# Optimization experiments

Hardware: AMD Instinct MI355X
Metric: run time of the kernel (lower is better)

## Reference

```python
import jax, jax.numpy as jnp
import numpy as np

D_K = 1024
NHEADS = 16
HEAD_DIM = D_K // NHEADS  # 64
STD = float(np.sqrt(HEAD_DIM))  # matches math.sqrt(d_k // nheads)


def setup_inputs() -> dict:
    key = jax.random.key(0)
    ks = jax.random.split(key, 9)
    B, S = 2, 2048
    scale = 1.0 / np.sqrt(D_K)
    x = jax.random.normal(ks[0], (B, S, D_K), dtype=jnp.float32)
    Wq = jax.random.normal(ks[1], (D_K, D_K), dtype=jnp.float32) * scale
    bq = jnp.zeros((D_K,), dtype=jnp.float32)
    Wk = jax.random.normal(ks[2], (D_K, D_K), dtype=jnp.float32) * scale
    bk = jnp.zeros((D_K,), dtype=jnp.float32)
    Wv = jax.random.normal(ks[3], (D_K, D_K), dtype=jnp.float32) * scale
    bv = jnp.zeros((D_K,), dtype=jnp.float32)
    Wo = jax.random.normal(ks[4], (D_K, D_K), dtype=jnp.float32) * scale
    bo = jnp.zeros((D_K,), dtype=jnp.float32)
    return {"x": x, "Wq": Wq, "bq": bq, "Wk": Wk, "bk": bk,
            "Wv": Wv, "bv": bv, "Wo": Wo, "bo": bo}


def _heads(x, W, b):
    # Linear then split heads: (B,S,D) -> (B,H,S,hd)
    B, S, _ = x.shape
    out = x @ W.T + b
    return out.reshape(B, S, NHEADS, HEAD_DIM).transpose(0, 2, 1, 3)


def reference(x, Wq, bq, Wk, bk, Wv, bv, Wo, bo):
    B, S, _ = x.shape
    q = _heads(x, Wq, bq)  # (B,H,S,hd)
    k = _heads(x, Wk, bk)
    v = _heads(x, Wv, bv)
    scores = jnp.einsum('bhqd,bhkd->bhqk', q, k) / STD  # (B,H,S,S)
    causal = jnp.tril(jnp.ones((S, S), dtype=bool))  # mask_factory default
    scores = jnp.where(causal[None, None, :, :], scores, -jnp.inf)
    attn = jax.nn.softmax(scores, axis=-1)
    ctx = jnp.einsum('bhqk,bhkd->bhqd', attn, v)  # (B,H,S,hd)
    ctx = ctx.transpose(0, 2, 1, 3).reshape(B, S, D_K)
    return ctx @ Wo.T + bo
```

## Files before the change

kernel.cpp:

```cpp
#include <hip/hip_runtime.h>
#include <stdint.h>

typedef unsigned short u16;
typedef __bf16 bf16x8 __attribute__((ext_vector_type(8)));
typedef __bf16 bf16x4v __attribute__((ext_vector_type(4)));
typedef float f32x4 __attribute__((ext_vector_type(4)));

typedef __attribute__((address_space(3))) uint32_t lds_u32;
typedef __attribute__((address_space(1))) uint32_t glb_u32;

__device__ __forceinline__ f32x4 mfma16(bf16x8 a, bf16x8 b, f32x4 c) {
    return __builtin_amdgcn_mfma_f32_16x16x32_bf16(a, b, c, 0, 0, 0);
}

__device__ __forceinline__ ushort4 pk4(float a, float b, float c, float d) {
    bf16x4v v;
    v[0] = (__bf16)a; v[1] = (__bf16)b; v[2] = (__bf16)c; v[3] = (__bf16)d;
    union { bf16x4v v; ushort4 u; } cv; cv.v = v; return cv.u;
}

__device__ __forceinline__ float fexp2(float x) {
    return __builtin_amdgcn_exp2f(x);
}

__device__ __forceinline__ void async16(const u16* g, u16* l) {
    __builtin_amdgcn_global_load_lds((glb_u32*)(uintptr_t)(const void*)g,
                                     (lds_u32*)l, 16, 0, 0);
}

__global__ __launch_bounds__(256) void cast_all(
    const float* __restrict__ x,
    const float* __restrict__ w0, const float* __restrict__ w1,
    const float* __restrict__ w2, const float* __restrict__ w3,
    u16* __restrict__ xo, u16* __restrict__ o0, u16* __restrict__ o1,
    u16* __restrict__ o2, u16* __restrict__ o3)
{
    const int s = blockIdx.y;
    const int i = (blockIdx.x * 256 + threadIdx.x) * 4;
    if (s == 0) {
#pragma unroll
        for (int c = 0; c < 4; ++c) {
            const int j = i + c * (1 << 20);
            float4 v = *(const float4*)(x + j);
            *(ushort4*)(xo + j) = pk4(v.x, v.y, v.z, v.w);
        }
    } else {
        const float* in = s == 1 ? w0 : (s == 2 ? w1 : (s == 3 ? w2 : w3));
        u16* out       = s == 1 ? o0 : (s == 2 ? o1 : (s == 3 ? o2 : o3));
        float4 v = *(const float4*)(in + i);
        *(ushort4*)(out + i) = pk4(v.x, v.y, v.z, v.w);
    }
}

__global__ __launch_bounds__(256) void gemm_qkv(
    const u16* __restrict__ A,
    const u16* __restrict__ W0, const u16* __restrict__ W1, const u16* __restrict__ W2,
    const float* __restrict__ B0, const float* __restrict__ B1, const float* __restrict__ B2,
    u16* __restrict__ O0, u16* __restrict__ O1,
    u16* __restrict__ VT,
    int M, int N, int K)
{
    const int x = blockIdx.x & 7;
    const int L = blockIdx.x >> 3;
    const int tm = (8 * (x >> 1) + (L & 7)) << 7;
    const int tnsel = 12 * (x & 1) + (L >> 3);
    const int sel = tnsel >> 3;
    const int tn  = (tnsel & 7) << 7;

    const u16* W      = sel == 0 ? W0 : (sel == 1 ? W1 : W2);
    const float* bias = sel == 0 ? B0 : (sel == 1 ? B1 : B2);
    u16* O            = sel == 0 ? O0 : O1;

    __shared__ __attribute__((aligned(16))) u16 As[128 * 64];
    __shared__ __attribute__((aligned(16))) u16 Bs[128 * 64];
    u16 (*Tb)[136] = (u16 (*)[136])As;

    const int tid  = threadIdx.x;
    const int lane = tid & 63;
    const int w    = tid >> 6;
    const int l15  = lane & 15;
    const int quad = lane >> 4;

    const int wm = (w >> 1) << 6;
    const int wn = (w & 1) << 6;

    f32x4 acc[4][4];
#pragma unroll
    for (int i = 0; i < 4; ++i)
#pragma unroll
        for (int j = 0; j < 4; ++j) acc[i][j] = f32x4{0.f, 0.f, 0.f, 0.f};

    const int lr  = lane >> 3;
    const int lcc = lane & 7;
    const int scc = lcc ^ lr;
    const u16* Ag = A + (size_t)(tm + 32 * w + lr) * K + scc * 8;
    const u16* Wg = W + (size_t)(tn + 32 * w + lr) * K + scc * 8;
    u16* Al = &As[(32 * w + lr) * 64 + lcc * 8];
    u16* Bl = &Bs[(32 * w + lr) * 64 + lcc * 8];

    for (int k0 = 0; k0 < K; k0 += 64) {
        __syncthreads();
#pragma unroll
        for (int m = 0; m < 4; ++m) {
            async16(Ag + k0 + (size_t)m * 8 * K, Al + m * 512);
            async16(Wg + k0 + (size_t)m * 8 * K, Bl + m * 512);
        }
        asm volatile("s_waitcnt vmcnt(0)" ::: "memory");
        __syncthreads();

#pragma unroll
        for (int kk = 0; kk < 2; ++kk) {
            bf16x8 a[4], b[4];
#pragma unroll
            for (int i = 0; i < 4; ++i) {
                const int r  = wm + 16 * i + l15;
                const int sl = (kk * 4 + quad) ^ (r & 7);
                a[i] = *(const bf16x8*)&As[r * 64 + sl * 8];
            }
#pragma unroll
            for (int j = 0; j < 4; ++j) {
                const int r  = wn + 16 * j + l15;
                const int sl = (kk * 4 + quad) ^ (r & 7);
                b[j] = *(const bf16x8*)&Bs[r * 64 + sl * 8];
            }
#pragma unroll
            for (int i = 0; i < 4; ++i)
#pragma unroll
                for (int j = 0; j < 4; ++j)
                    acc[i][j] = mfma16(a[i], b[j], acc[i][j]);
        }
    }

    if (sel == 2) {
        const int bb = tm >> 11;
        const int s0 = tm & 2047;
        const size_t vtb = ((size_t)bb << 10) + tn;
        for (int c32 = 0; c32 < 128; c32 += 32) {
            __syncthreads();
            if ((c32 >> 6) == (wn >> 6)) {
                const int j0 = (c32 >> 4) & 2;
#pragma unroll
                for (int jj = 0; jj < 2; ++jj) {
                    const int j  = j0 + jj;
                    const int cc = jj * 16 + l15;
                    const float bj = bias[tn + wn + 16 * j + l15];
#pragma unroll
                    for (int i = 0; i < 4; ++i) {
                        const int rr = wm + 16 * i + quad * 4;
                        *(ushort4*)&Tb[cc][rr] =
                            pk4(acc[i][j][0] + bj, acc[i][j][1] + bj,
                                acc[i][j][2] + bj, acc[i][j][3] + bj);
                    }
                }
            }
            __syncthreads();
            {
                const int c  = tid >> 3;
                const int ss = (tid & 7) * 16;
                uint4 v0 = *(const uint4*)&Tb[c][ss];
                uint4 v1 = *(const uint4*)&Tb[c][ss + 8];
                u16* dst = &VT[(vtb + c32 + c) * 2048 + s0 + ss];
                *(uint4*)dst       = v0;
                *(uint4*)(dst + 8) = v1;
            }
        }
    } else {
#pragma unroll
        for (int j = 0; j < 4; ++j) {
            const int col = tn + wn + 16 * j + l15;
            const float bj = bias[col];
#pragma unroll
            for (int i = 0; i < 4; ++i) {
                const int row = tm + wm + 16 * i + quad * 4;
#pragma unroll
                for (int r = 0; r < 4; ++r) {
                    union { float f; unsigned u; } v; v.f = acc[i][j][r] + bj;
                    unsigned rn = v.u + 0x7FFFu + ((v.u >> 16) & 1u);
                    O[(size_t)(row + r) * N + col] = (u16)(rn >> 16);
                }
            }
        }
    }
}

__global__ __launch_bounds__(256) void gemm_out64(
    const u16* __restrict__ A, const u16* __restrict__ W,
    const float* __restrict__ bias, float* __restrict__ O,
    int M, int N, int K)
{
    __shared__ __attribute__((aligned(16))) u16 As[128 * 64];
    __shared__ __attribute__((aligned(16))) u16 Bs[64 * 64];

    const int x = blockIdx.x & 7;
    const int L = blockIdx.x >> 3;
    const int tm = (8 * (x >> 1) + (L & 7)) << 7;
    const int tn = (8 * (x & 1) + (L >> 3)) << 6;

    const int tid  = threadIdx.x;
    const int lane = tid & 63;
    const int w    = tid >> 6;
    const int l15  = lane & 15;
    const int quad = lane >> 4;

    const int wm = (w >> 1) << 6;
    const int wn = (w & 1) << 5;

    f32x4 acc[4][2];
#pragma unroll
    for (int i = 0; i < 4; ++i)
#pragma unroll
        for (int j = 0; j < 2; ++j) acc[i][j] = f32x4{0.f, 0.f, 0.f, 0.f};

    const int lr  = lane >> 3;
    const int lcc = lane & 7;
    const int scc = lcc ^ lr;
    const u16* Ag = A + (size_t)(tm + 32 * w + lr) * K + scc * 8;
    const u16* Wg = W + (size_t)(tn + 16 * w + lr) * K + scc * 8;
    u16* Al = &As[(32 * w + lr) * 64 + lcc * 8];
    u16* Bl = &Bs[(16 * w + lr) * 64 + lcc * 8];

    for (int k0 = 0; k0 < K; k0 += 64) {
        __syncthreads();
#pragma unroll
        for (int m = 0; m < 4; ++m)
            async16(Ag + k0 + (size_t)m * 8 * K, Al + m * 512);
#pragma unroll
        for (int m = 0; m < 2; ++m)
            async16(Wg + k0 + (size_t)m * 8 * K, Bl + m * 512);
        asm volatile("s_waitcnt vmcnt(0)" ::: "memory");
        __syncthreads();

#pragma unroll
        for (int kk = 0; kk < 2; ++kk) {
            bf16x8 a[4], b[2];
#pragma unroll
            for (int i = 0; i < 4; ++i) {
                const int r  = wm + 16 * i + l15;
                const int sl = (kk * 4 + quad) ^ (r & 7);
                a[i] = *(const bf16x8*)&As[r * 64 + sl * 8];
            }
#pragma unroll
            for (int j = 0; j < 2; ++j) {
                const int r  = wn + 16 * j + l15;
                const int sl = (kk * 4 + quad) ^ (r & 7);
                b[j] = *(const bf16x8*)&Bs[r * 64 + sl * 8];
            }
#pragma unroll
            for (int i = 0; i < 4; ++i)
#pragma unroll
                for (int j = 0; j < 2; ++j)
                    acc[i][j] = mfma16(a[i], b[j], acc[i][j]);
        }
    }

#pragma unroll
    for (int j = 0; j < 2; ++j) {
        const int col = tn + wn + 16 * j + l15;
        const float bj = bias[col];
#pragma unroll
        for (int i = 0; i < 4; ++i) {
            const int row = tm + wm + 16 * i + quad * 4;
#pragma unroll
            for (int r = 0; r < 4; ++r)
                O[(size_t)(row + r) * N + col] = acc[i][j][r] + bj;
        }
    }
}

__device__ __forceinline__ bf16x8 rdt(const u16* base, int t, int l15, int cc) {
    const int r = t * 16 + l15;
    const int c = (cc & 3) ^ ((r >> 1) & 3);
    return *(const bf16x8*)(base + (cc >> 2) * 2048 + r * 32 + c * 8);
}

#define QK_EXP(Z, PROW, QG, MASKED, RSV, KB)                                   \
    do {                                                                       \
        _Pragma("unroll")                                                      \
        for (int t = 0; t < 4; ++t) {                                          \
            float e0 = fexp2(fmaf((Z)[t][0], SC, -16.0f));                     \
            float e1 = fexp2(fmaf((Z)[t][1], SC, -16.0f));                     \
            float e2 = fexp2(fmaf((Z)[t][2], SC, -16.0f));                     \
            float e3 = fexp2(fmaf((Z)[t][3], SC, -16.0f));                     \
            if (MASKED) {                                                      \
                const int kb = (KB) + t * 16 + quad * 4;                       \
                if (kb + 0 > (QG)) e0 = 0.f;                                   \
                if (kb + 1 > (QG)) e1 = 0.f;                                   \
                if (kb + 2 > (QG)) e2 = 0.f;                                   \
                if (kb + 3 > (QG)) e3 = 0.f;                                   \
            }                                                                  \
            (RSV)[0] += e0; (RSV)[1] += e1;                                    \
            (RSV)[2] += e2; (RSV)[3] += e3;                                    \
            *(ushort4*)((PROW) + (((2 * t + whi) ^ sl7) << 3) + woff) =        \
                pk4(e0, e1, e2, e3);                                           \
        }                                                                      \
    } while (0)

__global__ __launch_bounds__(256) void attn7(
    const u16* __restrict__ Q, const u16* __restrict__ Kb,
    const u16* __restrict__ VT, u16* __restrict__ ctx)
{
    __shared__ __attribute__((aligned(16))) u16 Kt[2][4096];
    __shared__ __attribute__((aligned(16))) u16 Vt[2][4096];
    __shared__ __attribute__((aligned(16))) u16 Pt[4][32][64];

    const int tid  = threadIdx.x;
    const int lane = tid & 63;
    const int wid  = tid >> 6;
    const int l15  = lane & 15;
    const int quad = lane >> 4;
    const int sl7  = l15 & 7;
    const int whi  = quad >> 1;
    const int woff = (quad & 1) * 4;

    const int hb = blockIdx.x & 31;
    const int h  = hb & 15, b = hb >> 4;
    const int ti = blockIdx.x >> 5;
    const int g  = (ti & 1) ? (15 - (ti >> 1)) : (ti >> 1);

    const int sL = 4 * g + wid, sH = 127 - sL;
    const int KL = g, KH = 31 - g;

    const size_t rowbase = (size_t)b * 2048;
    const int cbase = h * 64;
    const u16* kbase = Kb + rowbase * 1024 + cbase;
    const u16* vbase = VT + ((size_t)b * 1024 + cbase) * 2048;

    const int qgL = sL * 16 + l15, qgH = sH * 16 + l15;
    const u16* qpL = Q + (rowbase + qgL) * 1024 + cbase + quad * 8;
    const u16* qpH = Q + (rowbase + qgH) * 1024 + cbase + quad * 8;
    const bf16x8 qL0 = *(const bf16x8*)qpL, qL1 = *(const bf16x8*)(qpL + 32);
    const bf16x8 qH0 = *(const bf16x8*)qpH, qH1 = *(const bf16x8*)(qpH + 32);

    const int sr  = tid >> 2;
    const int sc0 = (((tid & 3) ^ ((sr >> 1) & 3)) << 3);
    const u16* kg = kbase + (size_t)sr * 1024 + sc0;
    const u16* vg = vbase + (size_t)sr * 2048 + sc0;

    f32x4 oL[4], oH[4];
#pragma unroll
    for (int i = 0; i < 4; ++i) { oL[i] = f32x4{0,0,0,0}; oH[i] = f32x4{0,0,0,0}; }
    f32x4 rsLv = {0,0,0,0}, rsHv = {0,0,0,0};
    const float SC = 0.18033688011112042f;

    u16 (*ptw)[64] = Pt[wid];
    u16* const prH = &ptw[16 + l15][0];
    u16* const prL = &ptw[l15][0];

    async16(kg,      &Kt[0][tid * 8]);
    async16(kg + 32, &Kt[0][2048 + tid * 8]);
    async16(vg,      &Vt[0][tid * 8]);
    async16(vg + 32, &Vt[0][2048 + tid * 8]);

    for (int kt = 0; kt <= KH; ++kt) {
        const int cur = kt & 1, nxt = cur ^ 1;
        asm volatile("s_waitcnt vmcnt(0)" ::: "memory");
        __syncthreads();
        if (kt < KH) {
            const u16* kgn = kg + (size_t)(kt + 1) * 65536;
            const u16* vgn = vg + (kt + 1) * 64;
            async16(kgn,      &Kt[nxt][tid * 8]);
            async16(kgn + 32, &Kt[nxt][2048 + tid * 8]);
            async16(vgn,      &Vt[nxt][tid * 8]);
            async16(vgn + 32, &Vt[nxt][2048 + tid * 8]);
        }
        const u16* KT = Kt[cur];
        const u16* VL = Vt[cur];
        const bool doL = (kt <= KL);
        const bool mH = (kt == KH), mL = (kt == KL);

        f32x4 zH[4], zL[4];
        __builtin_amdgcn_s_setprio(1);
        if (doL) {
#pragma unroll
            for (int t = 0; t < 4; ++t) {
                const bf16x8 kA = rdt(KT, t, l15, quad);
                const bf16x8 kB = rdt(KT, t, l15, quad + 4);
                f32x4 zh = {0,0,0,0};
                zh = mfma16(kA, qH0, zh);
                zh = mfma16(kB, qH1, zh);
                zH[t] = zh;
                f32x4 zl = {0,0,0,0};
                zl = mfma16(kA, qL0, zl);
                zl = mfma16(kB, qL1, zl);
                zL[t] = zl;
            }
        } else {
#pragma unroll
            for (int t = 0; t < 4; ++t) {
                const bf16x8 kA = rdt(KT, t, l15, quad);
                const bf16x8 kB = rdt(KT, t, l15, quad + 4);
                f32x4 zh = {0,0,0,0};
                zh = mfma16(kA, qH0, zh);
                zh = mfma16(kB, qH1, zh);
                zH[t] = zh;
            }
        }
        __builtin_amdgcn_s_setprio(0);

        const int ktb = kt * 64;
        if (mH) QK_EXP(zH, prH, qgH, 1, rsHv, ktb);
        else    QK_EXP(zH, prH, qgH, 0, rsHv, ktb);
        if (doL) {
            if (mL) QK_EXP(zL, prL, qgL, 1, rsLv, ktb);
            else    QK_EXP(zL, prL, qgL, 0, rsLv, ktb);
        }

        const bf16x8 bH0 = *(const bf16x8*)(prH + ((quad ^ sl7) << 3));
        const bf16x8 bH1 = *(const bf16x8*)(prH + (((quad | 4) ^ sl7) << 3));
        if (doL) {
            const bf16x8 bL0 = *(const bf16x8*)(prL + ((quad ^ sl7) << 3));
            const bf16x8 bL1 = *(const bf16x8*)(prL + (((quad | 4) ^ sl7) << 3));
            __builtin_amdgcn_s_setprio(1);
#pragma unroll
            for (int t = 0; t < 4; ++t) {
                const bf16x8 vA = rdt(VL, t, l15, quad);
                const bf16x8 vB = rdt(VL, t, l15, quad + 4);
                oH[t] = mfma16(vA, bH0, oH[t]);
                oH[t] = mfma16(vB, bH1, oH[t]);
                oL[t] = mfma16(vA, bL0, oL[t]);
                oL[t] = mfma16(vB, bL1, oL[t]);
            }
            __builtin_amdgcn_s_setprio(0);
        } else {
            __builtin_amdgcn_s_setprio(1);
#pragma unroll
            for (int t = 0; t < 4; ++t) {
                const bf16x8 vA = rdt(VL, t, l15, quad);
                const bf16x8 vB = rdt(VL, t, l15, quad + 4);
                oH[t] = mfma16(vA, bH0, oH[t]);
                oH[t] = mfma16(vB, bH1, oH[t]);
            }
            __builtin_amdgcn_s_setprio(0);
        }
    }

    float rsH = (rsHv[0] + rsHv[1]) + (rsHv[2] + rsHv[3]);
    float rsL = (rsLv[0] + rsLv[1]) + (rsLv[2] + rsLv[3]);
    rsH += __shfl_xor(rsH, 16); rsH += __shfl_xor(rsH, 32);
    rsL += __shfl_xor(rsL, 16); rsL += __shfl_xor(rsL, 32);
    const float iH = 1.0f / rsH, iL = 1.0f / rsL;
#pragma unroll
    for (int t = 0; t < 4; ++t) {
        *(ushort4*)&ctx[(rowbase + qgL) * 1024 + cbase + t * 16 + quad * 4] =
            pk4(oL[t][0] * iL, oL[t][1] * iL, oL[t][2] * iL, oL[t][3] * iL);
        *(ushort4*)&ctx[(rowbase + qgH) * 1024 + cbase + t * 16 + quad * 4] =
            pk4(oH[t][0] * iH, oH[t][1] * iH, oH[t][2] * iH, oH[t][3] * iH);
    }
}

extern "C" void kernel_launch(void* const* d_in, const int* in_sizes, int n_in,
                              void* d_out, int out_size, void* d_ws, size_t ws_size,
                              hipStream_t stream) {
    const float* x  = (const float*)d_in[0];
    const float* Wq = (const float*)d_in[1];
    const float* bq = (const float*)d_in[2];
    const float* Wk = (const float*)d_in[3];
    const float* bk = (const float*)d_in[4];
    const float* Wv = (const float*)d_in[5];
    const float* bv = (const float*)d_in[6];
    const float* Wo = (const float*)d_in[7];
    const float* bo = (const float*)d_in[8];
    float* out = (float*)d_out;

    const int N = 1024, K = 1024;
    const int M = in_sizes[0] / K;
    const size_t MN = (size_t)M * N;
    const size_t WN = (size_t)N * K;

    u16* xb  = (u16*)d_ws;
    u16* wqb = xb  + MN;
    u16* wkb = wqb + WN;
    u16* wvb = wkb + WN;
    u16* wob = wvb + WN;
    u16* q   = wob + WN;
    u16* kb  = q   + MN;
    u16* vt  = kb  + MN;
    u16* ctx = q;

    cast_all<<<dim3(1024, 5), 256, 0, stream>>>(
        x, Wq, Wk, Wv, Wo, xb, wqb, wkb, wvb, wob);

    gemm_qkv<<<dim3(768), 256, 0, stream>>>(
        xb, wqb, wkb, wvb, bq, bk, bv, q, kb, vt, M, N, K);

    attn7<<<dim3(512), 256, 0, stream>>>(q, kb, vt, ctx);

    gemm_out64<<<dim3(512), 256, 0, stream>>>(
        ctx, wob, bo, out, M, N, K);
}
```

Baseline: 194.6 us.

## Software-pipeline attention by deferring PV MFMAs one tile to overlap with QK

Moves the P·V matrix products for key tile kt-1 into iteration kt, right after the Q·K MFMAs. This lets them overlap with the exp/softmax work of the current tile instead of waiting on the P LDS round trip. The P fragments are carried in registers across iterations. V gets a third LDS buffer so the previous tile stays valid while the next one is prefetched, and an epilogue handles the final tile. The cost is 8KB more shared memory and more live registers, which could lower occupancy.

```diff
diff --git a/kernel.cpp b/kernel.cpp
--- a/kernel.cpp
+++ b/kernel.cpp
@@ -295,12 +295,12 @@
         }                                                                      \
     } while (0)
 
-__global__ __launch_bounds__(256) void attn7(
+__global__ __launch_bounds__(256) void attn8(
     const u16* __restrict__ Q, const u16* __restrict__ Kb,
     const u16* __restrict__ VT, u16* __restrict__ ctx)
 {
     __shared__ __attribute__((aligned(16))) u16 Kt[2][4096];
-    __shared__ __attribute__((aligned(16))) u16 Vt[2][4096];
+    __shared__ __attribute__((aligned(16))) u16 Vt[3][4096];
     __shared__ __attribute__((aligned(16))) u16 Pt[4][32][64];
 
     const int tid  = threadIdx.x;
@@ -351,20 +351,25 @@
     async16(vg,      &Vt[0][tid * 8]);
     async16(vg + 32, &Vt[0][2048 + tid * 8]);
 
+    bf16x8 pbH0 = {}, pbH1 = {}, pbL0 = {}, pbL1 = {};
+    bool doLp = false;
+    int c3 = 0;
+
     for (int kt = 0; kt <= KH; ++kt) {
-        const int cur = kt & 1, nxt = cur ^ 1;
+        const int curK = kt & 1, nxtK = curK ^ 1;
+        const int n3 = (c3 == 2) ? 0 : c3 + 1;
+        const int p3 = 3 - c3 - n3;
         asm volatile("s_waitcnt vmcnt(0)" ::: "memory");
         __syncthreads();
         if (kt < KH) {
             const u16* kgn = kg + (size_t)(kt + 1) * 65536;
             const u16* vgn = vg + (kt + 1) * 64;
-            async16(kgn,      &Kt[nxt][tid * 8]);
-            async16(kgn + 32, &Kt[nxt][2048 + tid * 8]);
-            async16(vgn,      &Vt[nxt][tid * 8]);
-            async16(vgn + 32, &Vt[nxt][2048 + tid * 8]);
-        }
-        const u16* KT = Kt[cur];
-        const u16* VL = Vt[cur];
+            async16(kgn,      &Kt[nxtK][tid * 8]);
+            async16(kgn + 32, &Kt[nxtK][2048 + tid * 8]);
+            async16(vgn,      &Vt[n3][tid * 8]);
+            async16(vgn + 32, &Vt[n3][2048 + tid * 8]);
+        }
+        const u16* KT = Kt[curK];
         const bool doL = (kt <= KL);
         const bool mH = (kt == KH), mL = (kt == KL);
 
@@ -395,6 +400,28 @@
                 zH[t] = zh;
             }
         }
+        if (kt > 0) {
+            const u16* VP = Vt[p3];
+            if (doLp) {
+#pragma unroll
+                for (int t = 0; t < 4; ++t) {
+                    const bf16x8 vA = rdt(VP, t, l15, quad);
+                    const bf16x8 vB = rdt(VP, t, l15, quad + 4);
+                    oH[t] = mfma16(vA, pbH0, oH[t]);
+                    oH[t] = mfma16(vB, pbH1, oH[t]);
+                    oL[t] = mfma16(vA, pbL0, oL[t]);
+                    oL[t] = mfma16(vB, pbL1, oL[t]);
+                }
+            } else {
+#pragma unroll
+                for (int t = 0; t < 4; ++t) {
+                    const bf16x8 vA = rdt(VP, t, l15, quad);
+                    const bf16x8 vB = rdt(VP, t, l15, quad + 4);
+                    oH[t] = mfma16(vA, pbH0, oH[t]);
+                    oH[t] = mfma16(vB, pbH1, oH[t]);
+                }
+            }
+        }
         __builtin_amdgcn_s_setprio(0);
 
         const int ktb = kt * 64;
@@ -405,33 +432,28 @@
             else    QK_EXP(zL, prL, qgL, 0, rsLv, ktb);
         }
 
-        const bf16x8 bH0 = *(const bf16x8*)(prH + ((quad ^ sl7) << 3));
-        const bf16x8 bH1 = *(const bf16x8*)(prH + (((quad | 4) ^ sl7) << 3));
+        pbH0 = *(const bf16x8*)(prH + ((quad ^ sl7) << 3));
+        pbH1 = *(const bf16x8*)(prH + (((quad | 4) ^ sl7) << 3));
         if (doL) {
-            const bf16x8 bL0 = *(const bf16x8*)(prL + ((quad ^ sl7) << 3));
-            const bf16x8 bL1 = *(const bf16x8*)(prL + (((quad | 4) ^ sl7) << 3));
-            __builtin_amdgcn_s_setprio(1);
-#pragma unroll
-            for (int t = 0; t < 4; ++t) {
-                const bf16x8 vA = rdt(VL, t, l15, quad);
-                const bf16x8 vB = rdt(VL, t, l15, quad + 4);
-                oH[t] = mfma16(vA, bH0, oH[t]);
-                oH[t] = mfma16(vB, bH1, oH[t]);
-                oL[t] = mfma16(vA, bL0, oL[t]);
-                oL[t] = mfma16(vB, bL1, oL[t]);
-            }
-            __builtin_amdgcn_s_setprio(0);
-        } else {
-            __builtin_amdgcn_s_setprio(1);
-#pragma unroll
-            for (int t = 0; t < 4; ++t) {
-                const bf16x8 vA = rdt(VL, t, l15, quad);
-                const bf16x8 vB = rdt(VL, t, l15, quad + 4);
-                oH[t] = mfma16(vA, bH0, oH[t]);
-                oH[t] = mfma16(vB, bH1, oH[t]);
-            }
-            __builtin_amdgcn_s_setprio(0);
-        }
+            pbL0 = *(const bf16x8*)(prL + ((quad ^ sl7) << 3));
+            pbL1 = *(const bf16x8*)(prL + (((quad | 4) ^ sl7) << 3));
+        }
+        doLp = doL;
+        c3 = n3;
+    }
+
+    {
+        const int epi3 = (c3 == 0) ? 2 : c3 - 1;
+        const u16* VP = Vt[epi3];
+        __builtin_amdgcn_s_setprio(1);
+#pragma unroll
+        for (int t = 0; t < 4; ++t) {
+            const bf16x8 vA = rdt(VP, t, l15, quad);
+            const bf16x8 vB = rdt(VP, t, l15, quad + 4);
+            oH[t] = mfma16(vA, pbH0, oH[t]);
+            oH[t] = mfma16(vB, pbH1, oH[t]);
+        }
+        __builtin_amdgcn_s_setprio(0);
     }
 
     float rsH = (rsHv[0] + rsHv[1]) + (rsHv[2] + rsHv[3]);
@@ -483,7 +505,7 @@
     gemm_qkv<<<dim3(768), 256, 0, stream>>>(
         xb, wqb, wkb, wvb, bq, bk, bv, q, kb, vt, M, N, K);
 
-    attn7<<<dim3(512), 256, 0, stream>>>(q, kb, vt, ctx);
+    attn8<<<dim3(512), 256, 0, stream>>>(q, kb, vt, ctx);
 
     gemm_out64<<<dim3(512), 256, 0, stream>>>(
         ctx, wob, bo, out, M, N, K);
```

New measurement: 192.8 us. Within noise of the previous version (-0.9%).
